# Kernel optimization log

Measured on AMD Instinct MI355X. Metric: run time of the kernel, lower is better.

## Reference

```python
import jax, jax.numpy as jnp
import numpy as np

H = 300   # hidden_size
B = 2048  # number of graphs
L = 64    # max atoms per graph


def _ragged():
    sizes = 32 + (np.arange(B) % 33)          # sizes in [32, 64], deterministic
    starts = np.concatenate([[0], np.cumsum(sizes)[:-1]])
    N = int(sizes.sum())                       # 98273
    seg_id = np.repeat(np.arange(B), sizes)    # graph id per global node row
    offset = np.arange(N) - starts[seg_id]     # local position within graph
    return sizes, starts, N, seg_id, offset


def setup_inputs() -> dict:
    key = jax.random.key(0)
    sizes, starts, N, seg_id, offset = _ragged()
    ks = jax.random.split(key, 10)
    s = 1.0 / np.sqrt(H)
    u = lambda k, shp: jax.random.uniform(k, shp, jnp.float32, -s, s)
    return {
        "node": jax.random.normal(ks[0], (N, H), jnp.float32),
        "bias": u(ks[1], (H,)),
        "W_ih_f": u(ks[2], (3 * H, H)), "W_hh_f": u(ks[3], (3 * H, H)),
        "b_ih_f": u(ks[4], (3 * H,)), "b_hh_f": u(ks[5], (3 * H,)),
        "W_ih_b": u(ks[6], (3 * H, H)), "W_hh_b": u(ks[7], (3 * H, H)),
        "b_ih_b": u(ks[8], (3 * H,)), "b_hh_b": u(ks[9], (3 * H,)),
        "starts": jnp.asarray(starts, jnp.int32),
        "sizes": jnp.asarray(sizes, jnp.int32),
        "seg_id": jnp.asarray(seg_id, jnp.int32),
        "offset": jnp.asarray(offset, jnp.int32),
    }


def _gru_dir(x, h0, W_ih, W_hh, b_ih, b_hh, reverse):
    # x: [B, L, H], h0: [B, H]; torch nn.GRU cell math, one direction
    xp = jnp.einsum('blh,gh->blg', x, W_ih) + b_ih  # [B, L, 3H]

    def step(h, xt):
        gh = h @ W_hh.T + b_hh
        i_r, i_z, i_n = jnp.split(xt, 3, axis=-1)
        h_r, h_z, h_n = jnp.split(gh, 3, axis=-1)
        r = jax.nn.sigmoid(i_r + h_r)
        z = jax.nn.sigmoid(i_z + h_z)
        n = jnp.tanh(i_n + r * h_n)
        h_new = (1.0 - z) * n + z * h
        return h_new, h_new

    _, ys = jax.lax.scan(step, h0, jnp.swapaxes(xp, 0, 1), reverse=reverse)
    return jnp.swapaxes(ys, 0, 1)  # [B, L, H], time-aligned to input


def reference(node, bias, W_ih_f, W_hh_f, b_ih_f, b_hh_f,
              W_ih_b, W_hh_b, b_ih_b, b_hh_b,
              starts, sizes, seg_id, offset):
    N = node.shape[0]
    message = jax.nn.relu(node + bias)                       # [N, H]

    l_idx = jnp.arange(L)
    mask = l_idx[None, :] < sizes[:, None]                   # [B, L] valid positions
    idx = jnp.clip(starts[:, None] + l_idx[None, :], 0, N - 1)

    # pack: zero-padded per-graph message batch [B, L, H]
    padded = jnp.where(mask[..., None], message[idx], 0.0)
    # per-graph max-pool of raw hidden (node) -> h0 for both GRU directions
    hpool = jnp.max(jnp.where(mask[..., None], node[idx], -jnp.inf), axis=1)

    out_f = _gru_dir(padded, hpool, W_ih_f, W_hh_f, b_ih_f, b_hh_f, reverse=False)
    out_b = _gru_dir(padded, hpool, W_ih_b, W_hh_b, b_ih_b, b_hh_b, reverse=True)
    cur = jnp.concatenate([out_f, out_b], axis=-1)           # [B, L, 2H]

    # unpad back to flat node order
    unpad = cur[seg_id, offset]                              # [N, 2H]
    head = jnp.concatenate([message[:1], message[:1]], axis=1)  # [1, 2H]
    return jnp.concatenate([head, unpad], axis=0)            # [N+1, 2H]
```

## Files before the change

### kernel.cpp

```cpp
#include <hip/hip_runtime.h>
#include <math.h>

#define Hc 300
#define Ld 64
#define GB 16
#define GBF 16
#define KT 10
#define NQ 20
#define NT 60
#define PERDIR (2*2*KT*NT*64)
#define TOTF   (2*PERDIR)
#define NCW 10
#define NTH 768

typedef _Float16 f16x8 __attribute__((ext_vector_type(8)));
typedef float f32x4 __attribute__((ext_vector_type(4)));
typedef unsigned int u32;

#define MFMA16(a,b,c) __builtin_amdgcn_mfma_f32_16x16x32_f16(a,b,c,0,0,0)

__global__ __launch_bounds__(256) void k_prep(
    const float* __restrict__ Wih_f, const float* __restrict__ Whh_f,
    const float* __restrict__ Wih_b, const float* __restrict__ Whh_b,
    const float* __restrict__ bih_f, const float* __restrict__ bhh_f,
    const float* __restrict__ bih_b, const float* __restrict__ bhh_b,
    const float* __restrict__ node, const float* __restrict__ bias,
    f16x8* __restrict__ Bfrag, float* __restrict__ bcomb, float* __restrict__ out)
{
  int gid = blockIdx.x*256 + threadIdx.x;
  if (gid < TOTF) {
    int lane = gid & 63;
    int s = gid >> 6;
    int nt = s % NT;  s /= NT;
    int kt = s % KT;  s /= KT;
    int term = s & 1; s >>= 1;
    int gemm = s & 1; s >>= 1;
    int dir  = s;
    int sec = nt / NQ, qq = nt - sec*NQ;
    int c = qq*16 + (lane & 15);
    int row = sec*Hc + c;
    const float* W = dir ? (gemm ? Whh_b : Wih_b) : (gemm ? Whh_f : Wih_f);
    f16x8 v;
#pragma unroll
    for (int e = 0; e < 8; ++e) {
      int k = kt*32 + (lane>>4)*8 + e;
      float wv = (c < Hc && k < Hc) ? W[row*Hc + k] : 0.f;
      _Float16 hi = (_Float16)wv;
      v[e] = term ? (_Float16)(wv - (float)hi) : hi;
    }
    Bfrag[gid] = v;
    return;
  }
  int i = gid - TOTF;
  if (i < 2560) {
    int dir = i / 1280; int r = i - dir*1280;
    int buf = r / 320, c = r - buf*320;
    const float* bih = dir ? bih_b : bih_f;
    const float* bhh = dir ? bhh_b : bhh_f;
    float v = 0.f;
    if (c < Hc) {
      if (buf == 0) v = bih[c] + bhh[c];
      else if (buf == 1) v = bih[Hc+c] + bhh[Hc+c];
      else if (buf == 2) v = bih[2*Hc+c];
      else v = bhh[2*Hc+c];
    }
    bcomb[i] = v;
    return;
  }
  i -= 2560;
  if (i < 600) {
    int c = (i < Hc) ? i : i - Hc;
    out[i] = fmaxf(node[c] + bias[c], 0.f);
  }
}

__device__ __forceinline__ u32 f32_to_hl(float v) {
  union { _Float16 f; unsigned short u; } a, b;
  a.f = (_Float16)v;
  b.f = (_Float16)(v - (float)a.f);
  return (u32)a.u | ((u32)b.u << 16);
}

__device__ __forceinline__ float ntl1(const float* p) {
  return __builtin_nontemporal_load(p);
}
__device__ __forceinline__ f32x4 ntl4(const float* p) {
  return __builtin_nontemporal_load((const f32x4*)p);
}

__device__ __forceinline__ void gll16(const void* g, void* l) {
  __builtin_amdgcn_global_load_lds(
      (const __attribute__((address_space(1))) u32*)g,
      (__attribute__((address_space(3))) u32*)l, 16, 0, 0);
}

__device__ __forceinline__ void afh_write(u32 (&buf)[2][KT][256],
                                          int l15, int g, int cE, u32 p, int lane) {
  u32 qv = (u32)__builtin_amdgcn_ds_bpermute((lane ^ 1) << 2, (int)p);
  int kt = cE >> 5;
  int dw = ((((cE >> 3) & 3) << 4) + g) * 4 + ((cE & 7) >> 1);
  if ((l15 & 1) == 0) buf[0][kt][dw] = (p & 0xFFFFu) | (qv << 16);
  else                buf[1][kt][dw] = (qv >> 16) | (p & 0xFFFF0000u);
}

__device__ __forceinline__ float sigf(float x) {
  return __builtin_amdgcn_rcpf(1.f + __expf(-x));
}
__device__ __forceinline__ float tanhfast(float x) {
  return 1.f - 2.f * __builtin_amdgcn_rcpf(__expf(2.f * x) + 1.f);
}

__global__ __launch_bounds__(640) void k_xp(
    const float* __restrict__ node, const float* __restrict__ bias,
    const f16x8* __restrict__ Bfrag, float* __restrict__ xp, int Nrows)
{
  __shared__ __align__(16) u32 AfX[2][4][KT][256];
  int tid = threadIdx.x, w = tid >> 6, lane = tid & 63;
  int l15 = lane & 15, l4 = lane >> 4;
  int r0 = blockIdx.x * 64;

  int k8 = w*32 + (l4 << 3);
  float bb[8];
#pragma unroll
  for (int e = 0; e < 8; ++e) bb[e] = 0.f;
  if (k8 + 8 <= Hc) {
    f32x4 a = *(const f32x4*)&bias[k8];
    f32x4 b = *(const f32x4*)&bias[k8+4];
#pragma unroll
    for (int e = 0; e < 4; ++e) { bb[e] = a[e]; bb[e+4] = b[e]; }
  } else if (k8 < Hc) {
    f32x4 a = *(const f32x4*)&bias[k8];
#pragma unroll
    for (int e = 0; e < 4; ++e) bb[e] = a[e];
  }

#pragma unroll
  for (int mt = 0; mt < 4; ++mt) {
    int row = r0 + mt*16 + l15;
    float xv[8];
#pragma unroll
    for (int e = 0; e < 8; ++e) xv[e] = 0.f;
    if (row < Nrows) {
      const float* rp = node + (size_t)row * Hc + k8;
      if (k8 + 8 <= Hc) {
        f32x4 a = ntl4(rp);
        f32x4 b = ntl4(rp + 4);
#pragma unroll
        for (int e = 0; e < 4; ++e) {
          xv[e]   = fmaxf(a[e] + bb[e],   0.f);
          xv[e+4] = fmaxf(b[e] + bb[e+4], 0.f);
        }
      } else if (k8 < Hc) {
        f32x4 a = ntl4(rp);
#pragma unroll
        for (int e = 0; e < 4; ++e) xv[e] = fmaxf(a[e] + bb[e], 0.f);
      }
    }
    f16x8 vh, vl;
#pragma unroll
    for (int e = 0; e < 8; ++e) {
      vh[e] = (_Float16)xv[e];
      vl[e] = (_Float16)(xv[e] - (float)vh[e]);
    }
    *(f16x8*)&AfX[0][mt][w][lane*4] = vh;
    *(f16x8*)&AfX[1][mt][w][lane*4] = vl;
  }
  __syncthreads();

  int qv0 = w, qv1 = w + 10;
  int c0 = qv0*16 + l15, c1 = qv1*16 + l15;
  const f32x4 zz = {0.f, 0.f, 0.f, 0.f};

#pragma unroll 1
  for (int dir = 0; dir < 2; ++dir) {
    const f16x8* Bxh = Bfrag + (size_t)dir * PERDIR;

#pragma unroll 1
    for (int qi = 0; qi < 2; ++qi) {
      int qv = qi ? qv1 : qv0;
      int c  = qi ? c1  : c0;
      f32x4 acc[3][4];
#pragma unroll
      for (int sec = 0; sec < 3; ++sec)
#pragma unroll
        for (int mt = 0; mt < 4; ++mt) acc[sec][mt] = zz;

#pragma unroll 2
      for (int kt = 0; kt < KT; ++kt) {
        f16x8 axh[4], axl[4];
#pragma unroll
        for (int mt = 0; mt < 4; ++mt) {
          axh[mt] = *(const f16x8*)&AfX[0][mt][kt][lane*4];
          axl[mt] = *(const f16x8*)&AfX[1][mt][kt][lane*4];
        }
#pragma unroll
        for (int sec = 0; sec < 3; ++sec) {
          int nt = sec*NQ + qv;
          f16x8 bh = Bxh[(kt*NT + nt)*64 + lane];
#pragma unroll
          for (int mt = 0; mt < 4; ++mt) {
            acc[sec][mt] = MFMA16(axh[mt], bh, acc[sec][mt]);
            acc[sec][mt] = MFMA16(axl[mt], bh, acc[sec][mt]);
          }
        }
      }
      if (c < 304) {
#pragma unroll
        for (int sec = 0; sec < 3; ++sec)
#pragma unroll
          for (int mt = 0; mt < 4; ++mt)
#pragma unroll
            for (int j = 0; j < 4; ++j) {
              int row = r0 + mt*16 + (l4<<2) + j;
              if (row < Nrows)
                __builtin_nontemporal_store(acc[sec][mt][j],
                    &xp[((size_t)row*2 + dir)*912 + sec*304 + c]);
            }
      }
    }
  }
}

__global__ __launch_bounds__(NTH) void k_rec(
    const float* __restrict__ node,
    const f16x8* __restrict__ Bfrag, const float* __restrict__ bcomb,
    const float* __restrict__ xp,
    const int* __restrict__ starts, const int* __restrict__ sizes,
    float* __restrict__ out)
{
  __shared__ __align__(16) u32 Bbuf[2][15360];
  __shared__ __align__(16) u32 AfH[2][KT][256];
  __shared__ int sst[16], ssz[16];

  int bid = blockIdx.x;
  int dir = (bid & 7) >= 4;
  int tslot = (bid & 3) + (bid >> 3) * 4;
  int g0 = tslot * GB;

  int tid = threadIdx.x;
  int w = tid >> 6, lane = tid & 63;
  int l15 = lane & 15, l4 = lane >> 4;

  if (tid < 16) { sst[tid] = starts[g0 + tid]; ssz[tid] = sizes[g0 + tid]; }

  const f16x8* Bhh = Bfrag + (size_t)dir * PERDIR + 2*KT*NT*64;
  const f32x4 zz = {0.f, 0.f, 0.f, 0.f};

  bool prod = (w >= NCW);
  int pw = w - NCW;

  int qv0 = w, qv1 = w + 10;
  int c0 = qv0*16 + l15, c1 = qv1*16 + l15;

  const float* bc = bcomb + dir*1280;
  float bcr[2], bcz[2], bci[2], bch[2];
  float hreg0[4], hreg1[4];

  if (prod) {
#pragma unroll
    for (int ff = 0; ff < 30; ++ff) {
      int f = pw*30 + ff;
      const f16x8* gs = Bhh + ((size_t)(0*NT + (ff%3)*NQ + (pw*10 + ff/3)))*64 + lane;
      gll16((const void*)gs, (void*)((char*)&Bbuf[0][0] + f*1024));
    }
    asm volatile("s_waitcnt vmcnt(0)" ::: "memory");
  } else {
    bcr[0] = bc[c0];       bcr[1] = bc[c1];
    bcz[0] = bc[320 + c0]; bcz[1] = bc[320 + c1];
    bci[0] = bc[640 + c0]; bci[1] = bc[640 + c1];
    bch[0] = bc[960 + c0]; bch[1] = bc[960 + c1];
  }
  __syncthreads();

  if (!prod) {
#pragma unroll
    for (int j = 0; j < 4; ++j) {
      int g = (l4<<2) + j;
      int st = sst[g], sz = ssz[g];
      float m0 = -1e30f, m1 = 0.f;
      for (int i = 0; i < sz; ++i)
        m0 = fmaxf(m0, ntl1(&node[(size_t)(st + i) * Hc + c0]));
      if (c1 < Hc) {
        m1 = -1e30f;
        for (int i = 0; i < sz; ++i)
          m1 = fmaxf(m1, ntl1(&node[(size_t)(st + i) * Hc + c1]));
      }
      hreg0[j] = m0;
      hreg1[j] = m1;
      afh_write(AfH, l15, g, c0 & ~1, f32_to_hl(m0), lane);
      afh_write(AfH, l15, g, c1 & ~1, f32_to_hl(m1), lane);
    }
  }
  __syncthreads();

#pragma unroll 1
  for (int t = 0; t < Ld; ++t) {
    int time = dir ? (Ld-1-t) : t;

    float xvv0[3][4], xvv1[3][4];
    if (!prod) {
#pragma unroll
      for (int j = 0; j < 4; ++j) {
        int g = (l4<<2) + j;
        bool v = (time < ssz[g]);
        const float* xb = xp + ((size_t)(sst[g] + time)*2 + dir)*912 + c0;
#pragma unroll
        for (int sec = 0; sec < 3; ++sec)
          xvv0[sec][j] = v ? ntl1(xb + sec*304) : 0.f;
        bool v1 = (c1 < 304) && v;
        const float* xb1 = xp + ((size_t)(sst[g] + time)*2 + dir)*912 + c1;
#pragma unroll
        for (int sec = 0; sec < 3; ++sec)
          xvv1[sec][j] = v1 ? ntl1(xb1 + sec*304) : 0.f;
      }
    }

    f32x4 ha0[3] = { zz, zz, zz };
    f32x4 ha1[3] = { zz, zz, zz };

#pragma unroll 1
    for (int kt = 0; kt < KT; ++kt) {
      if (prod) {
        int nkt = (kt + 1 == KT) ? 0 : kt + 1;
        char* base = (char*)&Bbuf[(kt + 1) & 1][0];
#pragma unroll
        for (int ff = 0; ff < 30; ++ff) {
          int f = pw*30 + ff;
          const f16x8* gs = Bhh + ((size_t)(nkt*NT + (ff%3)*NQ + (pw*10 + ff/3)))*64 + lane;
          gll16((const void*)gs, (void*)(base + f*1024));
        }
        asm volatile("s_waitcnt vmcnt(0)" ::: "memory");
      } else {
        const char* bbase = (const char*)&Bbuf[kt & 1][0] + lane*16;
        f16x8 ah = *(const f16x8*)&AfH[0][kt][lane*4];
        f16x8 al = *(const f16x8*)&AfH[1][kt][lane*4];
#pragma unroll
        for (int sec = 0; sec < 3; ++sec) {
          f16x8 b0 = *(const f16x8*)(bbase + (qv0*3 + sec)*1024);
          ha0[sec] = MFMA16(ah, b0, ha0[sec]);
          ha0[sec] = MFMA16(al, b0, ha0[sec]);
          f16x8 b1 = *(const f16x8*)(bbase + (qv1*3 + sec)*1024);
          ha1[sec] = MFMA16(ah, b1, ha1[sec]);
          ha1[sec] = MFMA16(al, b1, ha1[sec]);
        }
      }
      __syncthreads();
    }

    if (!prod) {
#pragma unroll
      for (int j = 0; j < 4; ++j) {
        int g = (l4<<2) + j;
        float rr = sigf(ha0[0][j] + xvv0[0][j] + bcr[0]);
        float zi = sigf(ha0[1][j] + xvv0[1][j] + bcz[0]);
        float nn = tanhfast(xvv0[2][j] + bci[0] + rr * (ha0[2][j] + bch[0]));
        float h_ = (1.f - zi) * nn + zi * hreg0[j];
        hreg0[j] = h_;
        if (time < ssz[g])
          __builtin_nontemporal_store(h_,
              &out[(size_t)(1 + sst[g] + time)*600 + dir*Hc + c0]);
        afh_write(AfH, l15, g, c0 & ~1, f32_to_hl(h_), lane);

        float rr1 = sigf(ha1[0][j] + xvv1[0][j] + bcr[1]);
        float zi1 = sigf(ha1[1][j] + xvv1[1][j] + bcz[1]);
        float nn1 = tanhfast(xvv1[2][j] + bci[1] + rr1 * (ha1[2][j] + bch[1]));
        float h1 = (1.f - zi1) * nn1 + zi1 * hreg1[j];
        if (c1 >= Hc) h1 = 0.f;
        hreg1[j] = h1;
        if (c1 < Hc && time < ssz[g])
          __builtin_nontemporal_store(h1,
              &out[(size_t)(1 + sst[g] + time)*600 + dir*Hc + c1]);
        afh_write(AfH, l15, g, c1 & ~1, f32_to_hl(h1), lane);
      }
    }
    __syncthreads();
  }
}

__global__ __launch_bounds__(640) void k_rec_fb(
    const float* __restrict__ node, const float* __restrict__ bias,
    const f16x8* __restrict__ Bfrag, const float* __restrict__ bcomb,
    const int* __restrict__ starts, const int* __restrict__ sizes,
    float* __restrict__ out)
{
  __shared__ __align__(16) u32 AfX[2][4][KT][256];
  __shared__ __align__(16) u32 AfH[2][2][KT][256];
  __shared__ int sst[GBF], ssz[GBF];

  int bid = blockIdx.x;
  int dir = (bid & 7) >= 4;
  int tslot = (bid & 3) + (bid >> 3) * 4;
  int g0 = tslot * GBF;

  int tid = threadIdx.x;
  int w = tid >> 6, lane = tid & 63;
  int l15 = lane & 15, l4 = lane >> 4;

  if (tid < GBF) { sst[tid] = starts[g0 + tid]; ssz[tid] = sizes[g0 + tid]; }
  __syncthreads();

  int qv[2] = { w, w + 10 };
  int cq[2] = { qv[0]*16 + l15, qv[1]*16 + l15 };

  const float* bc = bcomb + dir*1280;
  float bcr[2], bcz[2], bci[2], bch[2];
#pragma unroll
  for (int qi = 0; qi < 2; ++qi) {
    int c = cq[qi];
    bcr[qi] = bc[c]; bcz[qi] = bc[320 + c]; bci[qi] = bc[640 + c]; bch[qi] = bc[960 + c];
  }
  int stj[4], szj[4];
#pragma unroll
  for (int j = 0; j < 4; ++j) { stj[j] = sst[(l4<<2)+j]; szj[j] = ssz[(l4<<2)+j]; }
  int stG = sst[l15], szG = ssz[l15];

  const f16x8* Bd  = Bfrag + (size_t)dir * PERDIR;
  const f16x8* Bxh = Bd;
  const f16x8* Bxl = Bd + KT*NT*64;
  const f16x8* Bhh = Bd + 2*KT*NT*64;
  const f16x8* Bhl = Bd + 3*KT*NT*64;
  const f32x4 zz = {0.f, 0.f, 0.f, 0.f};

  int k8 = w*32 + (l4<<3);
  float bb[8];
#pragma unroll
  for (int e = 0; e < 8; ++e) bb[e] = 0.f;
  if (k8 + 8 <= Hc) {
    f32x4 a = *(const f32x4*)&bias[k8];
    f32x4 b = *(const f32x4*)&bias[k8+4];
#pragma unroll
    for (int e = 0; e < 4; ++e) { bb[e] = a[e]; bb[e+4] = b[e]; }
  } else if (k8 < Hc) {
    f32x4 a = *(const f32x4*)&bias[k8];
#pragma unroll
    for (int e = 0; e < 4; ++e) bb[e] = a[e];
  }

  float hreg[2][4];
#pragma unroll
  for (int qi = 0; qi < 2; ++qi) {
    int c = cq[qi];
#pragma unroll
    for (int j = 0; j < 4; ++j) {
      float m = 0.f;
      if (c < Hc) {
        m = -1e30f;
        int st = stj[j], sz = szj[j];
        for (int i = 0; i < sz; ++i)
          m = fmaxf(m, node[(size_t)(st + i) * Hc + c]);
      }
      hreg[qi][j] = m;
      afh_write(AfH[0], l15, (l4<<2)+j, c & ~1, f32_to_hl(m), lane);
    }
  }

#define HSTEPF(S) { \
    constexpr int CUR = (S)&1; \
    constexpr int NXT = CUR^1; \
    f32x4 ha[2][3]; \
    _Pragma("unroll") \
    for (int qi = 0; qi < 2; ++qi) { ha[qi][0] = zz; ha[qi][1] = zz; ha[qi][2] = zz; } \
    _Pragma("unroll 2") \
    for (int kt = 0; kt < KT; ++kt) { \
      f16x8 ahh = *(const f16x8*)&AfH[CUR][0][kt][lane*4]; \
      f16x8 ahl = *(const f16x8*)&AfH[CUR][1][kt][lane*4]; \
      _Pragma("unroll") \
      for (int qi = 0; qi < 2; ++qi) { \
        _Pragma("unroll") \
        for (int sec = 0; sec < 3; ++sec) { \
          int nt = sec*NQ + qv[qi]; \
          f16x8 bh = Bhh[(kt*NT + nt)*64 + lane]; \
          f16x8 bl = Bhl[(kt*NT + nt)*64 + lane]; \
          ha[qi][sec] = MFMA16(ahh, bh, ha[qi][sec]); \
          ha[qi][sec] = MFMA16(ahh, bl, ha[qi][sec]); \
          ha[qi][sec] = MFMA16(ahl, bh, ha[qi][sec]); \
        } \
      } \
    } \
    int tt = 4*T + (S); \
    int time = dir ? (Ld-1-tt) : tt; \
    _Pragma("unroll") \
    for (int qi = 0; qi < 2; ++qi) { \
      int c = cq[qi]; \
      _Pragma("unroll") \
      for (int j = 0; j < 4; ++j) { \
        float rp_ = ha[qi][0][j] + xa[qi][0][S][j] + bcr[qi]; \
        float zp_ = ha[qi][1][j] + xa[qi][1][S][j] + bcz[qi]; \
        float r_ = 1.f/(1.f + __expf(-rp_)); \
        float z_ = 1.f/(1.f + __expf(-zp_)); \
        float n_ = tanhf(xa[qi][2][S][j] + bci[qi] + r_*(ha[qi][2][j] + bch[qi])); \
        float h_ = (1.f - z_)*n_ + z_*hreg[qi][j]; \
        if (c >= Hc) h_ = 0.f; \
        hreg[qi][j] = h_; \
        if (c < Hc && time < szj[j]) \
          out[(size_t)(1 + stj[j] + time)*600 + dir*Hc + c] = h_; \
        afh_write(AfH[NXT], l15, (l4<<2)+j, c & ~1, f32_to_hl(h_), lane); \
      } \
    } \
    __syncthreads(); \
  }

#pragma unroll 1
  for (int T = 0; T < Ld/4; ++T) {
#pragma unroll
    for (int s = 0; s < 4; ++s) {
      int tt = 4*T + s;
      int time = dir ? (Ld-1-tt) : tt;
      float xv[8];
#pragma unroll
      for (int e = 0; e < 8; ++e) xv[e] = 0.f;
      if (time < szG) {
        const float* rp = node + (size_t)(stG + time) * Hc + k8;
        if (k8 + 8 <= Hc) {
          f32x4 a = *(const f32x4*)rp;
          f32x4 b = *(const f32x4*)(rp + 4);
#pragma unroll
          for (int e = 0; e < 4; ++e) {
            xv[e]   = fmaxf(a[e] + bb[e],   0.f);
            xv[e+4] = fmaxf(b[e] + bb[e+4], 0.f);
          }
        } else if (k8 < Hc) {
          f32x4 a = *(const f32x4*)rp;
#pragma unroll
          for (int e = 0; e < 4; ++e) xv[e] = fmaxf(a[e] + bb[e], 0.f);
        }
      }
      f16x8 vh, vl;
#pragma unroll
      for (int e = 0; e < 8; ++e) {
        vh[e] = (_Float16)xv[e];
        vl[e] = (_Float16)(xv[e] - (float)vh[e]);
      }
      *(f16x8*)&AfX[0][s][w][lane*4] = vh;
      *(f16x8*)&AfX[1][s][w][lane*4] = vl;
    }
    __syncthreads();

    f32x4 xa[2][3][4];
#pragma unroll
    for (int qi = 0; qi < 2; ++qi)
#pragma unroll
      for (int sec = 0; sec < 3; ++sec)
#pragma unroll
        for (int mt = 0; mt < 4; ++mt) xa[qi][sec][mt] = zz;

#pragma unroll 1
    for (int kt = 0; kt < KT; ++kt) {
      f16x8 axh[4], axl[4];
#pragma unroll
      for (int mt = 0; mt < 4; ++mt) {
        axh[mt] = *(const f16x8*)&AfX[0][mt][kt][lane*4];
        axl[mt] = *(const f16x8*)&AfX[1][mt][kt][lane*4];
      }
#pragma unroll
      for (int qi = 0; qi < 2; ++qi) {
#pragma unroll
        for (int sec = 0; sec < 3; ++sec) {
          int nt = sec*NQ + qv[qi];
          f16x8 bh = Bxh[(kt*NT + nt)*64 + lane];
          f16x8 bl = Bxl[(kt*NT + nt)*64 + lane];
#pragma unroll
          for (int mt = 0; mt < 4; ++mt) {
            xa[qi][sec][mt] = MFMA16(axh[mt], bh, xa[qi][sec][mt]);
            xa[qi][sec][mt] = MFMA16(axh[mt], bl, xa[qi][sec][mt]);
            xa[qi][sec][mt] = MFMA16(axl[mt], bh, xa[qi][sec][mt]);
          }
        }
      }
    }

    HSTEPF(0)
    HSTEPF(1)
    HSTEPF(2)
    HSTEPF(3)
  }
#undef HSTEPF
}

extern "C" void kernel_launch(void* const* d_in, const int* in_sizes, int n_in,
                              void* d_out, int out_size, void* d_ws, size_t ws_size,
                              hipStream_t stream) {
  const float* node  = (const float*)d_in[0];
  const float* bias  = (const float*)d_in[1];
  const float* Wih_f = (const float*)d_in[2];
  const float* Whh_f = (const float*)d_in[3];
  const float* bih_f = (const float*)d_in[4];
  const float* bhh_f = (const float*)d_in[5];
  const float* Wih_b = (const float*)d_in[6];
  const float* Whh_b = (const float*)d_in[7];
  const float* bih_b = (const float*)d_in[8];
  const float* bhh_b = (const float*)d_in[9];
  const int* starts  = (const int*)d_in[10];
  const int* sizes   = (const int*)d_in[11];

  int ngr = in_sizes[10];
  int N = in_sizes[0] / Hc;

  float* out = (float*)d_out;
  f16x8* Bfrag = (f16x8*)d_ws;
  float* bcomb = (float*)((char*)d_ws + (size_t)TOTF*16);
  size_t xp_off = (size_t)TOTF*16 + 2560*4;
  size_t need = xp_off + (size_t)N * 1824 * 4;

  int prep_threads = TOTF + 2560 + 600;
  hipLaunchKernelGGL(k_prep, dim3((prep_threads + 255)/256), dim3(256), 0, stream,
                     Wih_f, Whh_f, Wih_b, Whh_b, bih_f, bhh_f, bih_b, bhh_b,
                     node, bias, Bfrag, bcomb, out);

  if (ws_size >= need && (ngr % GB) == 0) {
    float* xp = (float*)((char*)d_ws + xp_off);
    int nxb = (N + 63) / 64;
    hipLaunchKernelGGL(k_xp, dim3(nxb), dim3(640), 0, stream,
                       node, bias, Bfrag, xp, N);
    int ntile = ngr / GB;
    hipLaunchKernelGGL(k_rec, dim3(2*ntile), dim3(NTH), 0, stream,
                       node, Bfrag, bcomb, xp, starts, sizes, out);
  } else {
    int ntilef = ngr / GBF;
    hipLaunchKernelGGL(k_rec_fb, dim3(2*ntilef), dim3(640), 0, stream,
                       node, bias, Bfrag, bcomb, starts, sizes, out);
  }
}
```

Measured before the change: 1.400 ms.

## Deepen W_hh LDS pipeline to four half-stage buffers with relaxed waitcnt

The recurrent kernel's producer waves now stream W_hh fragments into four half-sized LDS buffers, keeping three stages in flight. They wait with vmcnt(30) instead of draining all loads before each barrier. Each kt iteration is split into two half-steps, one per column group, and __syncthreads is replaced with raw s_barrier plus explicit lgkmcnt waits and sched_barriers. The aim is to hide global-load latency behind the consumers' MFMA work. The cost is twice as many barriers per step and fragile manual waitcnt accounting.

```diff
diff --git a/kernel.cpp b/kernel.cpp
--- a/kernel.cpp
+++ b/kernel.cpp
@@ -18,6 +18,7 @@
 typedef unsigned int u32;
 
 #define MFMA16(a,b,c) __builtin_amdgcn_mfma_f32_16x16x32_f16(a,b,c,0,0,0)
+#define RBAR() do { __builtin_amdgcn_sched_barrier(0); __builtin_amdgcn_s_barrier(); __builtin_amdgcn_sched_barrier(0); } while (0)
 
 __global__ __launch_bounds__(256) void k_prep(
     const float* __restrict__ Wih_f, const float* __restrict__ Whh_f,
@@ -228,7 +229,7 @@
     const int* __restrict__ starts, const int* __restrict__ sizes,
     float* __restrict__ out)
 {
-  __shared__ __align__(16) u32 Bbuf[2][15360];
+  __shared__ __align__(16) u32 Bbuf[4][7680];
   __shared__ __align__(16) u32 AfH[2][KT][256];
   __shared__ int sst[16], ssz[16];
 
@@ -256,21 +257,29 @@
   float bcr[2], bcz[2], bci[2], bch[2];
   float hreg0[4], hreg1[4];
 
+#define PISSUE(U) { \
+    int kt_ = (U) >> 1, hf_ = (U) & 1; \
+    char* sb_ = ((char*)&Bbuf[0][0]) + ((U) & 3) * 30720; \
+    _Pragma("unroll") \
+    for (int ff = 0; ff < 15; ++ff) { \
+      int fi_ = pw*15 + ff; \
+      int q3_ = fi_ / 3; \
+      int sec_ = fi_ - 3*q3_; \
+      const f16x8* gs_ = Bhh + ((size_t)(kt_*NT + sec_*NQ + hf_*10 + q3_))*64 + lane; \
+      gll16((const void*)gs_, (void*)(sb_ + fi_*1024)); \
+    } }
+
   if (prod) {
-#pragma unroll
-    for (int ff = 0; ff < 30; ++ff) {
-      int f = pw*30 + ff;
-      const f16x8* gs = Bhh + ((size_t)(0*NT + (ff%3)*NQ + (pw*10 + ff/3)))*64 + lane;
-      gll16((const void*)gs, (void*)((char*)&Bbuf[0][0] + f*1024));
-    }
-    asm volatile("s_waitcnt vmcnt(0)" ::: "memory");
+    PISSUE(0) PISSUE(1) PISSUE(2)
+    asm volatile("s_waitcnt vmcnt(30)" ::: "memory");
   } else {
     bcr[0] = bc[c0];       bcr[1] = bc[c1];
     bcz[0] = bc[320 + c0]; bcz[1] = bc[320 + c1];
     bci[0] = bc[640 + c0]; bci[1] = bc[640 + c1];
     bch[0] = bc[960 + c0]; bch[1] = bc[960 + c1];
   }
-  __syncthreads();
+  asm volatile("s_waitcnt lgkmcnt(0)" ::: "memory");
+  RBAR();
 
   if (!prod) {
 #pragma unroll
@@ -291,7 +300,8 @@
       afh_write(AfH, l15, g, c1 & ~1, f32_to_hl(m1), lane);
     }
   }
-  __syncthreads();
+  asm volatile("s_waitcnt lgkmcnt(0)" ::: "memory");
+  RBAR();
 
 #pragma unroll 1
   for (int t = 0; t < Ld; ++t) {
@@ -321,30 +331,38 @@
 #pragma unroll 1
     for (int kt = 0; kt < KT; ++kt) {
       if (prod) {
-        int nkt = (kt + 1 == KT) ? 0 : kt + 1;
-        char* base = (char*)&Bbuf[(kt + 1) & 1][0];
-#pragma unroll
-        for (int ff = 0; ff < 30; ++ff) {
-          int f = pw*30 + ff;
-          const f16x8* gs = Bhh + ((size_t)(nkt*NT + (ff%3)*NQ + (pw*10 + ff/3)))*64 + lane;
-          gll16((const void*)gs, (void*)(base + f*1024));
-        }
-        asm volatile("s_waitcnt vmcnt(0)" ::: "memory");
+        int u3 = 2*kt + 3; if (u3 >= 20) u3 -= 20;
+        PISSUE(u3)
+        asm volatile("s_waitcnt vmcnt(30)" ::: "memory");
       } else {
-        const char* bbase = (const char*)&Bbuf[kt & 1][0] + lane*16;
+        const char* bbase = (const char*)&Bbuf[0][0] + ((2*kt) & 3)*30720 + lane*16;
         f16x8 ah = *(const f16x8*)&AfH[0][kt][lane*4];
         f16x8 al = *(const f16x8*)&AfH[1][kt][lane*4];
 #pragma unroll
         for (int sec = 0; sec < 3; ++sec) {
-          f16x8 b0 = *(const f16x8*)(bbase + (qv0*3 + sec)*1024);
+          f16x8 b0 = *(const f16x8*)(bbase + (w*3 + sec)*1024);
           ha0[sec] = MFMA16(ah, b0, ha0[sec]);
           ha0[sec] = MFMA16(al, b0, ha0[sec]);
-          f16x8 b1 = *(const f16x8*)(bbase + (qv1*3 + sec)*1024);
+        }
+      }
+      RBAR();
+
+      if (prod) {
+        int u4 = 2*kt + 4; if (u4 >= 20) u4 -= 20;
+        PISSUE(u4)
+        asm volatile("s_waitcnt vmcnt(30)" ::: "memory");
+      } else {
+        const char* bbase = (const char*)&Bbuf[0][0] + ((2*kt+1) & 3)*30720 + lane*16;
+        f16x8 ah = *(const f16x8*)&AfH[0][kt][lane*4];
+        f16x8 al = *(const f16x8*)&AfH[1][kt][lane*4];
+#pragma unroll
+        for (int sec = 0; sec < 3; ++sec) {
+          f16x8 b1 = *(const f16x8*)(bbase + (w*3 + sec)*1024);
           ha1[sec] = MFMA16(ah, b1, ha1[sec]);
           ha1[sec] = MFMA16(al, b1, ha1[sec]);
         }
       }
-      __syncthreads();
+      RBAR();
     }
 
     if (!prod) {
@@ -373,8 +391,10 @@
         afh_write(AfH, l15, g, c1 & ~1, f32_to_hl(h1), lane);
       }
     }
-    __syncthreads();
-  }
+    asm volatile("s_waitcnt lgkmcnt(0)" ::: "memory");
+    RBAR();
+  }
+#undef PISSUE
 }
 
 __global__ __launch_bounds__(640) void k_rec_fb(
```

Result: faster. 1.365 ms (median of 2 runs) (-2.5%).
